# Optimization experiments

Measured on AMD Instinct MI355X. Metric: run time of the kernel, lower is better.

The kernel has to match this reference:

```python
import jax, jax.numpy as jnp
import numpy as np

D_MODEL = 512
CONTEXT_LENGTH = 128


def setup_inputs() -> dict:
    key = jax.random.key(0)
    k1, k2, k3, k4 = jax.random.split(key, 4)
    B, T, C = 512, 128, D_MODEL
    H = 64  # head_size
    x = jax.random.normal(k1, (B, T, C), dtype=jnp.float32)
    # torch nn.Linear(d_model, head_size, bias=False) stores weight as [head_size, d_model]
    s = 1.0 / np.sqrt(C)
    Wq = jax.random.uniform(k2, (H, C), dtype=jnp.float32, minval=-s, maxval=s)
    Wk = jax.random.uniform(k3, (H, C), dtype=jnp.float32, minval=-s, maxval=s)
    Wv = jax.random.uniform(k4, (H, C), dtype=jnp.float32, minval=-s, maxval=s)
    return {"x": x, "Wq": Wq, "Wk": Wk, "Wv": Wv}


def reference(x, Wq, Wk, Wv):
    # x: [B, T, C]; Wq/Wk/Wv: [H, C] (torch Linear weight layout, y = x @ W^T)
    B, T, C = x.shape
    H = Wq.shape[0]
    Q = jnp.einsum('btc,hc->bth', x, Wq)  # [B, T, H]
    K = jnp.einsum('btc,hc->bth', x, Wk)
    V = jnp.einsum('btc,hc->bth', x, Wv)
    scale = 1.0 / jnp.sqrt(jnp.asarray(H, dtype=x.dtype))
    scores = jnp.einsum('bth,bsh->bts', Q, K) * scale  # [B, T, T]
    causal = jnp.tril(jnp.ones((T, T), dtype=bool))
    scores = jnp.where(causal, scores, jnp.asarray(-jnp.inf, dtype=scores.dtype))
    weights = jax.nn.softmax(scores, axis=-1)
    # dropout is identity in eval mode (reference baseline)
    out = jnp.einsum('bts,bsh->bth', weights, V)  # [B, T, H]
    return out
```

## Files before the change

kernel.cpp:

```cpp
#include <hip/hip_runtime.h>
#include <hip/hip_bf16.h>


#define TT 128
#define CC 512
#define HH 64

typedef __attribute__((ext_vector_type(8))) short bf16x8;
typedef __attribute__((ext_vector_type(4))) ushort u16x4;
typedef __attribute__((ext_vector_type(4))) float f32x4;

__device__ __forceinline__ ushort f2bf(float f) {
    union { float f; unsigned u; } v; v.f = f;
    unsigned r = v.u + 0x7fffu + ((v.u >> 16) & 1u);
    return (ushort)(r >> 16);
}

__device__ __forceinline__ void gload_lds16(const void* g, void* l) {
    __builtin_amdgcn_global_load_lds(
        (const __attribute__((address_space(1))) unsigned int*)g,
        (__attribute__((address_space(3))) unsigned int*)l, 16, 0, 0);
}

__global__ void wpack_kernel(const float* __restrict__ wq,
                             const float* __restrict__ wk,
                             const float* __restrict__ wv,
                             ushort* __restrict__ wpk) {
    int p = blockIdx.x * 256 + threadIdx.x;
    int j  = p & 7;
    int l  = (p >> 3) & 63;
    int nt = (p >> 9) % 12;
    int kt = p / (12 * 512);
    int w  = nt >> 2;
    const float* src = (w == 0) ? wq : ((w == 1) ? wk : wv);
    int h = (nt & 3) * 16 + (l & 15);
    int c = kt * 32 + ((l >> 4) << 3) + j;
    wpk[kt * 8192 + ((nt * 64 + l) * 8) + j] = f2bf(src[h * 512 + c]);
}

__launch_bounds__(512, 4)
__global__ void attn_fused_kernel(const float* __restrict__ x,
                                  const ushort* __restrict__ wpk,
                                  float* __restrict__ out) {
    __shared__ __align__(16) char smem[81920];
    ushort* ps  = (ushort*)smem;
    ushort* qs  = (ushort*)(smem + 32768);
    ushort* ks  = (ushort*)(smem + 49152);
    ushort* vst = (ushort*)(smem + 65536);

    const int tid  = threadIdx.x;
    const int wave = tid >> 6;
    const int lane = tid & 63;
    const int lq   = lane >> 4;
    const int lr   = lane & 15;
    const int b    = blockIdx.x;
    const size_t bB = (size_t)b * TT;

    const f32x4 fzero = {0.f, 0.f, 0.f, 0.f};

    f32x4 acc[12];
    #pragma unroll
    for (int j = 0; j < 12; ++j) acc[j] = fzero;

    const int r = wave * 16 + lr;
    const float* xr = x + (bB + r) * CC + lq * 8;

    auto stageW = [&](int kt, int s) {
        const char* wsrc = (const char*)wpk + kt * 16384;
        char* wdst = smem + s * 16384;
        #pragma unroll
        for (int p = 0; p < 2; ++p) {
            int off = wave * 2048 + p * 1024;
            gload_lds16(wsrc + off + lane * 16, wdst + off);
        }
    };

    #define LOADX(kt, dlo, dhi)                                                \
        {                                                                      \
            const float* p0 = xr + (kt) * 32;                                  \
            asm volatile("global_load_dwordx4 %0, %1, off"                     \
                         : "=&v"(dlo) : "v"(p0) : "memory");                   \
            asm volatile("global_load_dwordx4 %0, %1, off offset:16"           \
                         : "=&v"(dhi) : "v"(p0) : "memory");                   \
        }

    f32x4 x0a, x0b, x1a, x1b, x2a, x2b;

    stageW(0, 0);
    LOADX(0, x0a, x0b);
    LOADX(1, x1a, x1b);

    #pragma unroll
    for (int kt = 0; kt < 16; ++kt) {
        const int cur = kt % 3;

        __builtin_amdgcn_s_barrier();

        if (kt + 1 < 16) stageW(kt + 1, (kt + 1) & 1);
        if (kt + 2 < 16) {
            const int slot = (kt + 2) % 3;
            if (slot == 0)      LOADX(kt + 2, x0a, x0b)
            else if (slot == 1) LOADX(kt + 2, x1a, x1b)
            else                LOADX(kt + 2, x2a, x2b)
        }

        if (kt <= 13)      asm volatile("s_waitcnt vmcnt(6)" ::: "memory");
        else if (kt == 14) asm volatile("s_waitcnt vmcnt(4)" ::: "memory");
        else               asm volatile("s_waitcnt vmcnt(0)" ::: "memory");
        __builtin_amdgcn_sched_barrier(0);

        __builtin_amdgcn_s_barrier();
        __builtin_amdgcn_sched_barrier(0);

        f32x4 alo, ahi;
        if (cur == 0)      { alo = x0a; ahi = x0b; }
        else if (cur == 1) { alo = x1a; ahi = x1b; }
        else               { alo = x2a; ahi = x2b; }
        bf16x8 a;
        a[0] = (short)f2bf(alo[0]); a[1] = (short)f2bf(alo[1]);
        a[2] = (short)f2bf(alo[2]); a[3] = (short)f2bf(alo[3]);
        a[4] = (short)f2bf(ahi[0]); a[5] = (short)f2bf(ahi[1]);
        a[6] = (short)f2bf(ahi[2]); a[7] = (short)f2bf(ahi[3]);

        const ushort* wf = (const ushort*)(smem + (kt & 1) * 16384);
        bf16x8 w[12];
        #pragma unroll
        for (int nt = 0; nt < 12; ++nt)
            w[nt] = *(const bf16x8*)(wf + (nt * 64 + lane) * 8);
        #pragma unroll
        for (int nt = 0; nt < 12; ++nt)
            acc[nt] = __builtin_amdgcn_mfma_f32_16x16x32_bf16(a, w[nt], acc[nt], 0, 0, 0);
    }

    {
        const int t0 = wave * 16 + lq * 4;
        #pragma unroll
        for (int nt = 0; nt < 8; ++nt) {
            #pragma unroll
            for (int j = 0; j < 4; ++j) {
                int t = t0 + j;
                int h = (nt & 3) * 16 + lr;
                ushort v = f2bf(acc[nt][j]);
                if (nt < 4) qs[t * 64 + (h ^ ((t & 7) << 3))] = v;
                else        ks[t * 64 + (h ^ ((t & 7) << 3))] = v;
            }
        }
        #pragma unroll
        for (int nt = 8; nt < 12; ++nt) {
            int h = (nt & 3) * 16 + lr;
            int base = t0 ^ ((h & 7) << 3);
            u16x4 v4;
            v4[0] = f2bf(acc[nt][0]); v4[1] = f2bf(acc[nt][1]);
            v4[2] = f2bf(acc[nt][2]); v4[3] = f2bf(acc[nt][3]);
            *(u16x4*)&vst[h * 128 + base] = v4;
        }
    }
    __syncthreads();

    const int row0 = wave * 16;
    f32x4 s[8];
    #pragma unroll
    for (int j = 0; j < 8; ++j) s[j] = fzero;

    #pragma unroll
    for (int kt = 0; kt < 2; ++kt) {
        int h0 = kt * 32 + lq * 8;
        int t  = row0 + lr;
        bf16x8 a = *(const bf16x8*)&qs[t * 64 + (h0 ^ ((t & 7) << 3))];
        bf16x8 kf[8];
        #pragma unroll
        for (int nt = 0; nt < 8; ++nt) {
            int sc = nt * 16 + lr;
            kf[nt] = *(const bf16x8*)&ks[sc * 64 + (h0 ^ ((sc & 7) << 3))];
        }
        #pragma unroll
        for (int nt = 0; nt < 8; ++nt)
            s[nt] = __builtin_amdgcn_mfma_f32_16x16x32_bf16(a, kf[nt], s[nt], 0, 0, 0);
    }

    float rinv[4];
    #pragma unroll
    for (int j = 0; j < 4; ++j) {
        int t = row0 + lq * 4 + j;
        float m = -1e30f;
        #pragma unroll
        for (int nt = 0; nt < 8; ++nt) {
            int sc = nt * 16 + lr;
            float v = s[nt][j] * 0.125f;
            v = (sc <= t) ? v : -1e30f;
            s[nt][j] = v;
            m = fmaxf(m, v);
        }
        m = fmaxf(m, __shfl_xor(m, 1));
        m = fmaxf(m, __shfl_xor(m, 2));
        m = fmaxf(m, __shfl_xor(m, 4));
        m = fmaxf(m, __shfl_xor(m, 8));
        float sum = 0.f;
        #pragma unroll
        for (int nt = 0; nt < 8; ++nt) {
            float p = __expf(s[nt][j] - m);
            s[nt][j] = p;
            sum += p;
        }
        sum += __shfl_xor(sum, 1);
        sum += __shfl_xor(sum, 2);
        sum += __shfl_xor(sum, 4);
        sum += __shfl_xor(sum, 8);
        rinv[j] = 1.0f / sum;
    }

    #pragma unroll
    for (int j = 0; j < 4; ++j) {
        int t = row0 + lq * 4 + j;
        #pragma unroll
        for (int nt = 0; nt < 8; ++nt) {
            int sc = nt * 16 + lr;
            ps[t * 128 + (sc ^ ((t & 7) << 3))] = f2bf(s[nt][j]);
        }
    }

    f32x4 o[4];
    #pragma unroll
    for (int j = 0; j < 4; ++j) o[j] = fzero;

    #pragma unroll
    for (int ksv = 0; ksv < 4; ++ksv) {
        int s0 = ksv * 32 + lq * 8;
        int t  = row0 + lr;
        bf16x8 a = *(const bf16x8*)&ps[t * 128 + (s0 ^ ((t & 7) << 3))];
        bf16x8 vf[4];
        #pragma unroll
        for (int nt = 0; nt < 4; ++nt) {
            int h = nt * 16 + lr;
            vf[nt] = *(const bf16x8*)&vst[h * 128 + (s0 ^ ((h & 7) << 3))];
        }
        #pragma unroll
        for (int nt = 0; nt < 4; ++nt)
            o[nt] = __builtin_amdgcn_mfma_f32_16x16x32_bf16(a, vf[nt], o[nt], 0, 0, 0);
    }

    float* ob = out + (size_t)b * (TT * HH);
    #pragma unroll
    for (int nt = 0; nt < 4; ++nt)
        #pragma unroll
        for (int j = 0; j < 4; ++j) {
            int t = row0 + lq * 4 + j;
            int h = nt * 16 + lr;
            ob[t * HH + h] = o[nt][j] * rinv[j];
        }
}

extern "C" void kernel_launch(void* const* d_in, const int* in_sizes, int n_in,
                              void* d_out, int out_size, void* d_ws, size_t ws_size,
                              hipStream_t stream) {
    const float* x  = (const float*)d_in[0];
    const float* wq = (const float*)d_in[1];
    const float* wk = (const float*)d_in[2];
    const float* wv = (const float*)d_in[3];
    float* o = (float*)d_out;
    ushort* wpk = (ushort*)d_ws;

    (void)in_sizes; (void)n_in; (void)out_size; (void)ws_size;

    wpack_kernel<<<384, 256, 0, stream>>>(wq, wk, wv, wpk);
    attn_fused_kernel<<<512, 512, 0, stream>>>(x, wpk, o);
}
```

Measured before the change: 39.27 us.

## Process two batches per block with a deeper, continuous weight/x prefetch pipeline

```diff
diff --git a/kernel.cpp b/kernel.cpp
--- a/kernel.cpp
+++ b/kernel.cpp
@@ -20,6 +20,24 @@
     __builtin_amdgcn_global_load_lds(
         (const __attribute__((address_space(1))) unsigned int*)g,
         (__attribute__((address_space(3))) unsigned int*)l, 16, 0, 0);
+}
+
+__device__ __forceinline__ void waitv(int n) {
+    switch (n) {
+    case 0:  asm volatile("s_waitcnt vmcnt(0)"  ::: "memory"); break;
+    case 2:  asm volatile("s_waitcnt vmcnt(2)"  ::: "memory"); break;
+    case 4:  asm volatile("s_waitcnt vmcnt(4)"  ::: "memory"); break;
+    case 6:  asm volatile("s_waitcnt vmcnt(6)"  ::: "memory"); break;
+    case 8:  asm volatile("s_waitcnt vmcnt(8)"  ::: "memory"); break;
+    case 10: asm volatile("s_waitcnt vmcnt(10)" ::: "memory"); break;
+    case 12: asm volatile("s_waitcnt vmcnt(12)" ::: "memory"); break;
+    case 14: asm volatile("s_waitcnt vmcnt(14)" ::: "memory"); break;
+    case 16: asm volatile("s_waitcnt vmcnt(16)" ::: "memory"); break;
+    case 18: asm volatile("s_waitcnt vmcnt(18)" ::: "memory"); break;
+    case 20: asm volatile("s_waitcnt vmcnt(20)" ::: "memory"); break;
+    default: asm volatile("s_waitcnt vmcnt(30)" ::: "memory"); break;
+    }
+    __builtin_amdgcn_sched_barrier(0);
 }
 
 __global__ void wpack_kernel(const float* __restrict__ wq,
@@ -38,36 +56,37 @@
     wpk[kt * 8192 + ((nt * 64 + l) * 8) + j] = f2bf(src[h * 512 + c]);
 }
 
-__launch_bounds__(512, 4)
+__constant__ const int kWX[32] = {8,10,12,14,14,14,14,14,14,14,14,14,14,14,14,14,
+                                  30,30,30,30,14,14,14,14,14,14,14,14,14,10,6,2};
+__constant__ const int kWW[32] = {16,18,20,14,14,14,14,14,14,14,14,14,14,14,14,14,
+                                  30,30,30,14,14,14,14,14,14,14,14,14,12,8,4,0};
+
+__launch_bounds__(512, 2)
 __global__ void attn_fused_kernel(const float* __restrict__ x,
                                   const ushort* __restrict__ wpk,
                                   float* __restrict__ out) {
-    __shared__ __align__(16) char smem[81920];
-    ushort* ps  = (ushort*)smem;
-    ushort* qs  = (ushort*)(smem + 32768);
-    ushort* ks  = (ushort*)(smem + 49152);
-    ushort* vst = (ushort*)(smem + 65536);
+    __shared__ __align__(16) char smem[147456];
+    ushort* qs  = (ushort*)(smem + 65536);
+    ushort* ks  = (ushort*)(smem + 81920);
+    ushort* vst = (ushort*)(smem + 98304);
+    ushort* ps  = (ushort*)(smem + 114688);
 
     const int tid  = threadIdx.x;
     const int wave = tid >> 6;
     const int lane = tid & 63;
     const int lq   = lane >> 4;
     const int lr   = lane & 15;
-    const int b    = blockIdx.x;
-    const size_t bB = (size_t)b * TT;
+    const int b0   = blockIdx.x * 2;
+    const int b1   = b0 + 1;
 
     const f32x4 fzero = {0.f, 0.f, 0.f, 0.f};
-
-    f32x4 acc[12];
-    #pragma unroll
-    for (int j = 0; j < 12; ++j) acc[j] = fzero;
-
     const int r = wave * 16 + lr;
-    const float* xr = x + (bB + r) * CC + lq * 8;
-
-    auto stageW = [&](int kt, int s) {
-        const char* wsrc = (const char*)wpk + kt * 16384;
-        char* wdst = smem + s * 16384;
+    const float* xr0 = x + ((size_t)b0 * TT + r) * CC + lq * 8;
+    const float* xr1 = x + ((size_t)b1 * TT + r) * CC + lq * 8;
+
+    auto stageW = [&](int c, int buf) {
+        const char* wsrc = (const char*)wpk + (c & 15) * 16384;
+        char* wdst = smem + buf * 16384;
         #pragma unroll
         for (int p = 0; p < 2; ++p) {
             int off = wave * 2048 + p * 1024;
@@ -75,179 +94,183 @@
         }
     };
 
-    #define LOADX(kt, dlo, dhi)                                                \
+    #define LOADX(c, dlo, dhi)                                                 \
         {                                                                      \
-            const float* p0 = xr + (kt) * 32;                                  \
+            const float* p0 = ((c) < 16 ? xr0 : xr1) + ((c) & 15) * 32;        \
             asm volatile("global_load_dwordx4 %0, %1, off"                     \
                          : "=&v"(dlo) : "v"(p0) : "memory");                   \
             asm volatile("global_load_dwordx4 %0, %1, off offset:16"           \
                          : "=&v"(dhi) : "v"(p0) : "memory");                   \
         }
 
-    f32x4 x0a, x0b, x1a, x1b, x2a, x2b;
-
-    stageW(0, 0);
-    LOADX(0, x0a, x0b);
-    LOADX(1, x1a, x1b);
-
-    #pragma unroll
-    for (int kt = 0; kt < 16; ++kt) {
-        const int cur = kt % 3;
-
-        __builtin_amdgcn_s_barrier();
-
-        if (kt + 1 < 16) stageW(kt + 1, (kt + 1) & 1);
-        if (kt + 2 < 16) {
-            const int slot = (kt + 2) % 3;
-            if (slot == 0)      LOADX(kt + 2, x0a, x0b)
-            else if (slot == 1) LOADX(kt + 2, x1a, x1b)
-            else                LOADX(kt + 2, x2a, x2b)
-        }
-
-        if (kt <= 13)      asm volatile("s_waitcnt vmcnt(6)" ::: "memory");
-        else if (kt == 14) asm volatile("s_waitcnt vmcnt(4)" ::: "memory");
-        else               asm volatile("s_waitcnt vmcnt(0)" ::: "memory");
-        __builtin_amdgcn_sched_barrier(0);
-
-        __builtin_amdgcn_s_barrier();
-        __builtin_amdgcn_sched_barrier(0);
-
-        f32x4 alo, ahi;
-        if (cur == 0)      { alo = x0a; ahi = x0b; }
-        else if (cur == 1) { alo = x1a; ahi = x1b; }
-        else               { alo = x2a; ahi = x2b; }
-        bf16x8 a;
-        a[0] = (short)f2bf(alo[0]); a[1] = (short)f2bf(alo[1]);
-        a[2] = (short)f2bf(alo[2]); a[3] = (short)f2bf(alo[3]);
-        a[4] = (short)f2bf(ahi[0]); a[5] = (short)f2bf(ahi[1]);
-        a[6] = (short)f2bf(ahi[2]); a[7] = (short)f2bf(ahi[3]);
-
-        const ushort* wf = (const ushort*)(smem + (kt & 1) * 16384);
-        bf16x8 w[12];
-        #pragma unroll
-        for (int nt = 0; nt < 12; ++nt)
-            w[nt] = *(const bf16x8*)(wf + (nt * 64 + lane) * 8);
-        #pragma unroll
-        for (int nt = 0; nt < 12; ++nt)
-            acc[nt] = __builtin_amdgcn_mfma_f32_16x16x32_bf16(a, w[nt], acc[nt], 0, 0, 0);
-    }
-
-    {
-        const int t0 = wave * 16 + lq * 4;
-        #pragma unroll
-        for (int nt = 0; nt < 8; ++nt) {
-            #pragma unroll
-            for (int j = 0; j < 4; ++j) {
-                int t = t0 + j;
-                int h = (nt & 3) * 16 + lr;
-                ushort v = f2bf(acc[nt][j]);
-                if (nt < 4) qs[t * 64 + (h ^ ((t & 7) << 3))] = v;
-                else        ks[t * 64 + (h ^ ((t & 7) << 3))] = v;
-            }
-        }
-        #pragma unroll
-        for (int nt = 8; nt < 12; ++nt) {
-            int h = (nt & 3) * 16 + lr;
-            int base = t0 ^ ((h & 7) << 3);
-            u16x4 v4;
-            v4[0] = f2bf(acc[nt][0]); v4[1] = f2bf(acc[nt][1]);
-            v4[2] = f2bf(acc[nt][2]); v4[3] = f2bf(acc[nt][3]);
-            *(u16x4*)&vst[h * 128 + base] = v4;
-        }
-    }
-    __syncthreads();
-
-    const int row0 = wave * 16;
-    f32x4 s[8];
-    #pragma unroll
-    for (int j = 0; j < 8; ++j) s[j] = fzero;
-
-    #pragma unroll
-    for (int kt = 0; kt < 2; ++kt) {
-        int h0 = kt * 32 + lq * 8;
-        int t  = row0 + lr;
-        bf16x8 a = *(const bf16x8*)&qs[t * 64 + (h0 ^ ((t & 7) << 3))];
-        bf16x8 kf[8];
-        #pragma unroll
-        for (int nt = 0; nt < 8; ++nt) {
-            int sc = nt * 16 + lr;
-            kf[nt] = *(const bf16x8*)&ks[sc * 64 + (h0 ^ ((sc & 7) << 3))];
-        }
-        #pragma unroll
-        for (int nt = 0; nt < 8; ++nt)
-            s[nt] = __builtin_amdgcn_mfma_f32_16x16x32_bf16(a, kf[nt], s[nt], 0, 0, 0);
-    }
-
-    float rinv[4];
-    #pragma unroll
-    for (int j = 0; j < 4; ++j) {
-        int t = row0 + lq * 4 + j;
-        float m = -1e30f;
-        #pragma unroll
-        for (int nt = 0; nt < 8; ++nt) {
-            int sc = nt * 16 + lr;
-            float v = s[nt][j] * 0.125f;
-            v = (sc <= t) ? v : -1e30f;
-            s[nt][j] = v;
-            m = fmaxf(m, v);
-        }
-        m = fmaxf(m, __shfl_xor(m, 1));
-        m = fmaxf(m, __shfl_xor(m, 2));
-        m = fmaxf(m, __shfl_xor(m, 4));
-        m = fmaxf(m, __shfl_xor(m, 8));
-        float sum = 0.f;
-        #pragma unroll
-        for (int nt = 0; nt < 8; ++nt) {
-            float p = __expf(s[nt][j] - m);
-            s[nt][j] = p;
-            sum += p;
-        }
-        sum += __shfl_xor(sum, 1);
-        sum += __shfl_xor(sum, 2);
-        sum += __shfl_xor(sum, 4);
-        sum += __shfl_xor(sum, 8);
-        rinv[j] = 1.0f / sum;
-    }
-
-    #pragma unroll
-    for (int j = 0; j < 4; ++j) {
-        int t = row0 + lq * 4 + j;
-        #pragma unroll
-        for (int nt = 0; nt < 8; ++nt) {
-            int sc = nt * 16 + lr;
-            ps[t * 128 + (sc ^ ((t & 7) << 3))] = f2bf(s[nt][j]);
-        }
-    }
-
-    f32x4 o[4];
-    #pragma unroll
-    for (int j = 0; j < 4; ++j) o[j] = fzero;
-
-    #pragma unroll
-    for (int ksv = 0; ksv < 4; ++ksv) {
-        int s0 = ksv * 32 + lq * 8;
-        int t  = row0 + lr;
-        bf16x8 a = *(const bf16x8*)&ps[t * 128 + (s0 ^ ((t & 7) << 3))];
-        bf16x8 vf[4];
-        #pragma unroll
-        for (int nt = 0; nt < 4; ++nt) {
-            int h = nt * 16 + lr;
-            vf[nt] = *(const bf16x8*)&vst[h * 128 + (s0 ^ ((h & 7) << 3))];
-        }
-        #pragma unroll
-        for (int nt = 0; nt < 4; ++nt)
-            o[nt] = __builtin_amdgcn_mfma_f32_16x16x32_bf16(a, vf[nt], o[nt], 0, 0, 0);
-    }
-
-    float* ob = out + (size_t)b * (TT * HH);
-    #pragma unroll
-    for (int nt = 0; nt < 4; ++nt)
+    f32x4 x0a, x0b, x1a, x1b, x2a, x2b, x3a, x3b;
+    f32x4 acc[12];
+
+    auto do_attn = [&](int b, float* ob) {
+        const int row0 = wave * 16;
+        f32x4 s[8];
+        #pragma unroll
+        for (int j = 0; j < 8; ++j) s[j] = fzero;
+        #pragma unroll
+        for (int kt2 = 0; kt2 < 2; ++kt2) {
+            int h0 = kt2 * 32 + lq * 8;
+            int t  = row0 + lr;
+            bf16x8 a = *(const bf16x8*)&qs[t * 64 + (h0 ^ ((t & 7) << 3))];
+            bf16x8 kf[8];
+            #pragma unroll
+            for (int nt = 0; nt < 8; ++nt) {
+                int sc = nt * 16 + lr;
+                kf[nt] = *(const bf16x8*)&ks[sc * 64 + (h0 ^ ((sc & 7) << 3))];
+            }
+            #pragma unroll
+            for (int nt = 0; nt < 8; ++nt)
+                s[nt] = __builtin_amdgcn_mfma_f32_16x16x32_bf16(a, kf[nt], s[nt], 0, 0, 0);
+        }
+        float rinv[4];
         #pragma unroll
         for (int j = 0; j < 4; ++j) {
             int t = row0 + lq * 4 + j;
-            int h = nt * 16 + lr;
-            ob[t * HH + h] = o[nt][j] * rinv[j];
-        }
+            float m = -1e30f;
+            #pragma unroll
+            for (int nt = 0; nt < 8; ++nt) {
+                int sc = nt * 16 + lr;
+                float v = s[nt][j] * 0.125f;
+                v = (sc <= t) ? v : -1e30f;
+                s[nt][j] = v;
+                m = fmaxf(m, v);
+            }
+            m = fmaxf(m, __shfl_xor(m, 1));
+            m = fmaxf(m, __shfl_xor(m, 2));
+            m = fmaxf(m, __shfl_xor(m, 4));
+            m = fmaxf(m, __shfl_xor(m, 8));
+            float sum = 0.f;
+            #pragma unroll
+            for (int nt = 0; nt < 8; ++nt) {
+                float p = __expf(s[nt][j] - m);
+                s[nt][j] = p;
+                sum += p;
+            }
+            sum += __shfl_xor(sum, 1);
+            sum += __shfl_xor(sum, 2);
+            sum += __shfl_xor(sum, 4);
+            sum += __shfl_xor(sum, 8);
+            rinv[j] = 1.0f / sum;
+        }
+        #pragma unroll
+        for (int j = 0; j < 4; ++j) {
+            int t = row0 + lq * 4 + j;
+            #pragma unroll
+            for (int nt = 0; nt < 8; ++nt) {
+                int sc = nt * 16 + lr;
+                ps[t * 128 + (sc ^ ((t & 7) << 3))] = f2bf(s[nt][j]);
+            }
+        }
+        f32x4 o[4];
+        #pragma unroll
+        for (int j = 0; j < 4; ++j) o[j] = fzero;
+        #pragma unroll
+        for (int ksv = 0; ksv < 4; ++ksv) {
+            int s0 = ksv * 32 + lq * 8;
+            int t  = row0 + lr;
+            bf16x8 a = *(const bf16x8*)&ps[t * 128 + (s0 ^ ((t & 7) << 3))];
+            bf16x8 vf[4];
+            #pragma unroll
+            for (int nt = 0; nt < 4; ++nt) {
+                int h = nt * 16 + lr;
+                vf[nt] = *(const bf16x8*)&vst[h * 128 + (s0 ^ ((h & 7) << 3))];
+            }
+            #pragma unroll
+            for (int nt = 0; nt < 4; ++nt)
+                o[nt] = __builtin_amdgcn_mfma_f32_16x16x32_bf16(a, vf[nt], o[nt], 0, 0, 0);
+        }
+        #pragma unroll
+        for (int nt = 0; nt < 4; ++nt)
+            #pragma unroll
+            for (int j = 0; j < 4; ++j) {
+                int t = row0 + lq * 4 + j;
+                int h = nt * 16 + lr;
+                ob[t * HH + h] = o[nt][j] * rinv[j];
+            }
+    };
+
+    stageW(0, 0); stageW(1, 1); stageW(2, 2);
+    LOADX(0, x0a, x0b); LOADX(1, x1a, x1b);
+    LOADX(2, x2a, x2b); LOADX(3, x3a, x3b);
+
+    #pragma unroll
+    for (int e = 0; e < 2; ++e) {
+        #pragma unroll
+        for (int j = 0; j < 12; ++j) acc[j] = fzero;
+
+        #pragma unroll
+        for (int k = 0; k < 16; ++k) {
+            const int c = e * 16 + k;
+            const int slot = c & 3;
+
+            __builtin_amdgcn_s_barrier();
+
+            if (c + 3 < 32) stageW(c + 3, (c + 3) & 3);
+
+            waitv(kWX[c]);
+            f32x4 alo, ahi;
+            if (slot == 0)      { alo = x0a; ahi = x0b; }
+            else if (slot == 1) { alo = x1a; ahi = x1b; }
+            else if (slot == 2) { alo = x2a; ahi = x2b; }
+            else                { alo = x3a; ahi = x3b; }
+            bf16x8 a;
+            a[0] = (short)f2bf(alo[0]); a[1] = (short)f2bf(alo[1]);
+            a[2] = (short)f2bf(alo[2]); a[3] = (short)f2bf(alo[3]);
+            a[4] = (short)f2bf(ahi[0]); a[5] = (short)f2bf(ahi[1]);
+            a[6] = (short)f2bf(ahi[2]); a[7] = (short)f2bf(ahi[3]);
+
+            if (c + 4 < 32) {
+                if (slot == 0)      LOADX(c + 4, x0a, x0b)
+                else if (slot == 1) LOADX(c + 4, x1a, x1b)
+                else if (slot == 2) LOADX(c + 4, x2a, x2b)
+                else                LOADX(c + 4, x3a, x3b)
+            }
+
+            waitv(kWW[c]);
+            __builtin_amdgcn_s_barrier();
+            __builtin_amdgcn_sched_barrier(0);
+
+            const ushort* wf = (const ushort*)(smem + (c & 3) * 16384);
+            bf16x8 w[12];
+            #pragma unroll
+            for (int nt = 0; nt < 12; ++nt)
+                w[nt] = *(const bf16x8*)(wf + (nt * 64 + lane) * 8);
+            #pragma unroll
+            for (int nt = 0; nt < 12; ++nt)
+                acc[nt] = __builtin_amdgcn_mfma_f32_16x16x32_bf16(a, w[nt], acc[nt], 0, 0, 0);
+        }
+
+        {
+            const int t0 = wave * 16 + lq * 4;
+            #pragma unroll
+            for (int nt = 0; nt < 8; ++nt)
+                #pragma unroll
+                for (int j = 0; j < 4; ++j) {
+                    int t = t0 + j;
+                    int h = (nt & 3) * 16 + lr;
+                    ushort v = f2bf(acc[nt][j]);
+                    if (nt < 4) qs[t * 64 + (h ^ ((t & 7) << 3))] = v;
+                    else        ks[t * 64 + (h ^ ((t & 7) << 3))] = v;
+                }
+            #pragma unroll
+            for (int nt = 8; nt < 12; ++nt) {
+                int h = (nt & 3) * 16 + lr;
+                int base = t0 ^ ((h & 7) << 3);
+                u16x4 v4;
+                v4[0] = f2bf(acc[nt][0]); v4[1] = f2bf(acc[nt][1]);
+                v4[2] = f2bf(acc[nt][2]); v4[3] = f2bf(acc[nt][3]);
+                *(u16x4*)&vst[h * 128 + base] = v4;
+            }
+        }
+        __syncthreads();
+
+        do_attn(e ? b1 : b0,
+                out + (size_t)(e ? b1 : b0) * (TT * HH));
+    }
 }
 
 extern "C" void kernel_launch(void* const* d_in, const int* in_sizes, int n_in,
@@ -263,5 +286,5 @@
     (void)in_sizes; (void)n_in; (void)out_size; (void)ws_size;
 
     wpack_kernel<<<384, 256, 0, stream>>>(wq, wk, wv, wpk);
-    attn_fused_kernel<<<512, 512, 0, stream>>>(x, wpk, o);
-}
+    attn_fused_kernel<<<256, 512, 0, stream>>>(x, wpk, o);
+}
```

Result: slower. 44.72 us (+13.9%).
